# Optimization experiments

Measured on AMD Instinct MI355X. Metric: run time of the kernel, lower is better.

## Reference

```python
import jax, jax.numpy as jnp
import numpy as np

B, S, D, H = 2, 2048, 1024, 16
DK = D // H  # 64
EPS = 1e-10
ROPE_BASE = 500000.0


def _rms_norm(x, w):
    # RMSNorm over last dim: w * x / sqrt(mean(x^2) + eps)
    return w * x * jax.lax.rsqrt(jnp.mean(x * x, axis=-1, keepdims=True) + EPS)


def _rope_tables(seq_len, dk):
    inv_freq = 1.0 / (ROPE_BASE ** (jnp.arange(0, dk, 2, dtype=jnp.float32) / dk))
    t = jnp.arange(seq_len, dtype=jnp.float32)
    freqs = jnp.outer(t, inv_freq)            # (S, dk/2)
    emb = jnp.concatenate([freqs, freqs], -1)  # (S, dk)
    return jnp.cos(emb), jnp.sin(emb)


def _rotate_half(x):
    x1, x2 = jnp.split(x, 2, axis=-1)
    return jnp.concatenate([-x2, x1], axis=-1)


def setup_inputs() -> dict:
    key = jax.random.key(0)
    ks = jax.random.split(key, 8)
    scale = 1.0 / np.sqrt(D)
    return {
        "q": jax.random.normal(ks[0], (B, S, D), jnp.float32),
        "k": jax.random.normal(ks[1], (B, S, D), jnp.float32),
        "v": jax.random.normal(ks[2], (B, S, D), jnp.float32),
        "Wq": jax.random.normal(ks[3], (D, D), jnp.float32) * scale,
        "Wk": jax.random.normal(ks[4], (D, D), jnp.float32) * scale,
        "Wv": jax.random.normal(ks[5], (D, D), jnp.float32) * scale,
        "Wo": jax.random.normal(ks[6], (D, D), jnp.float32) * scale,
        "q_norm_w": jnp.ones((DK,), jnp.float32) + 0.02 * jax.random.normal(ks[7], (DK,), jnp.float32),
        "k_norm_w": jnp.ones((DK,), jnp.float32),
    }


def reference(q, k, v, Wq, Wk, Wv, Wo, q_norm_w, k_norm_w):
    Bq, Sq, _ = q.shape
    # Projections (torch Linear: x @ W.T), split into heads -> (B, H, S, DK)
    def proj(x, W):
        return (x @ W.T).reshape(Bq, Sq, H, DK).transpose(0, 2, 1, 3)
    query, key_, value = proj(q, Wq), proj(k, Wk), proj(v, Wv)
    # Per-head QK RMSNorm
    query = _rms_norm(query, q_norm_w)
    key_ = _rms_norm(key_, k_norm_w)
    # RoPE
    cos, sin = _rope_tables(Sq, DK)  # (S, DK) each; broadcast over (B, H)
    query = query * cos + _rotate_half(query) * sin
    key_ = key_ * cos + _rotate_half(key_) * sin
    # Causal attention
    scale = 1.0 / np.sqrt(DK)
    scores = jnp.einsum("bhqd,bhkd->bhqk", query, key_) * scale
    causal = jnp.tril(jnp.ones((Sq, Sq), bool))
    scores = jnp.where(causal, scores, -jnp.inf)
    probs = jax.nn.softmax(scores, axis=-1)
    attn = jnp.einsum("bhqk,bhkd->bhqd", probs, value)
    # Merge heads and output projection
    attn = attn.transpose(0, 2, 1, 3).reshape(Bq, Sq, D)
    return attn @ Wo.T
```

## Files before the change

kernel.cpp:

```cpp
#include <hip/hip_runtime.h>
#include <hip/hip_bf16.h>
#include <math.h>

#define B_  2
#define S_  2048
#define D_  1024
#define H_  16
#define DK_ 64

typedef __attribute__((ext_vector_type(8))) short bf16x8;
typedef __attribute__((ext_vector_type(4))) float f32x4;

#define MFMA_BF16(a, b, c) __builtin_amdgcn_mfma_f32_16x16x32_bf16((a), (b), (c), 0, 0, 0)

#define QSCALE 0.18033688011112042f
#define ROPE_L2 0.591611512f

__device__ __forceinline__ unsigned short f2bf(float f) {
  unsigned int u = __float_as_uint(f);
  u += 0x7FFFu + ((u >> 16) & 1u);
  return (unsigned short)(u >> 16);
}

__device__ __forceinline__ void gl_lds16(const void* g, void* l) {
  __builtin_amdgcn_global_load_lds(
      (const __attribute__((address_space(1))) void*)g,
      (__attribute__((address_space(3))) void*)l, 16, 0, 0);
}

__device__ __forceinline__ int lsw(int row, int col) {
  return row * 64 + ((((col) >> 3) ^ (row & 7)) << 3) + (col & 7);
}

__global__ __launch_bounds__(256)
void cvt_bf16(const float* __restrict__ q, const float* __restrict__ k,
              const float* __restrict__ v, const float* __restrict__ wq,
              const float* __restrict__ wk, const float* __restrict__ wv,
              const float* __restrict__ wo,
              unsigned short* __restrict__ qb, unsigned short* __restrict__ kb,
              unsigned short* __restrict__ vb, unsigned short* __restrict__ wqb,
              unsigned short* __restrict__ wkb, unsigned short* __restrict__ wvb,
              unsigned short* __restrict__ wob) {
  const float* src; unsigned short* dst; int n;
  switch (blockIdx.y) {
    case 0: src = q;  dst = qb;  n = B_ * S_ * D_; break;
    case 1: src = k;  dst = kb;  n = B_ * S_ * D_; break;
    case 2: src = v;  dst = vb;  n = B_ * S_ * D_; break;
    case 3: src = wq; dst = wqb; n = D_ * D_; break;
    case 4: src = wk; dst = wkb; n = D_ * D_; break;
    case 5: src = wv; dst = wvb; n = D_ * D_; break;
    default: src = wo; dst = wob; n = D_ * D_; break;
  }
  const int i = (blockIdx.x * 256 + threadIdx.x) * 4;
  if (i >= n) return;
  float4 val = *(const float4*)&src[i];
  ushort4 r4;
  r4.x = f2bf(val.x); r4.y = f2bf(val.y); r4.z = f2bf(val.z); r4.w = f2bf(val.w);
  *(ushort4*)&dst[i] = r4;
}

__global__ __launch_bounds__(256)
void gemm_qkv(const unsigned short* __restrict__ qa, const unsigned short* __restrict__ ka,
              const unsigned short* __restrict__ va,
              const unsigned short* __restrict__ wq, const unsigned short* __restrict__ wk,
              const unsigned short* __restrict__ wv,
              unsigned short* __restrict__ Qo, unsigned short* __restrict__ Ko,
              unsigned short* __restrict__ Vto,
              const float* __restrict__ qnw, const float* __restrict__ knw) {
  __shared__ unsigned short As[2][128 * 32];
  __shared__ unsigned short Bs[2][128 * 32];
  const int z = blockIdx.z;
  const unsigned short* A = (z == 0) ? qa : (z == 1) ? ka : va;
  const unsigned short* W = (z == 0) ? wq : (z == 1) ? wk : wv;

  const int t = threadIdx.x, lane = t & 63, wave = t >> 6;
  const int l16 = lane & 15, quad = lane >> 4;
  const int wm = wave >> 1, wn = wave & 1;
  const int m0 = blockIdx.y * 128, j0 = blockIdx.x * 128;

  f32x4 acc[4][4];
#pragma unroll
  for (int i = 0; i < 4; ++i)
#pragma unroll
    for (int j = 0; j < 4; ++j) acc[i][j] = (f32x4)(0.0f);

  auto stage = [&](int kb, int buf) {
#pragma unroll
    for (int i = 0; i < 2; ++i) {
      const int c  = (wave * 2 + i) * 64 + lane;
      const int r  = c >> 2;
      const int co = (c & 3) * 8;
      gl_lds16(&A[(size_t)(m0 + r) * D_ + kb + co], &As[buf][(wave * 2 + i) * 512]);
      gl_lds16(&W[(size_t)(j0 + r) * D_ + kb + co], &Bs[buf][(wave * 2 + i) * 512]);
    }
  };

  stage(0, 0);
  for (int kb = 0; kb < D_; kb += 32) {
    const int buf = (kb >> 5) & 1;
    __syncthreads();
    if (kb + 32 < D_) stage(kb + 32, buf ^ 1);

    bf16x8 af[4], bfr[4];
#pragma unroll
    for (int mi = 0; mi < 4; ++mi)
      af[mi] = *(const bf16x8*)&As[buf][(wm * 64 + mi * 16 + l16) * 32 + quad * 8];
#pragma unroll
    for (int ni = 0; ni < 4; ++ni)
      bfr[ni] = *(const bf16x8*)&Bs[buf][(wn * 64 + ni * 16 + l16) * 32 + quad * 8];
#pragma unroll
    for (int mi = 0; mi < 4; ++mi)
#pragma unroll
      for (int ni = 0; ni < 4; ++ni)
        acc[mi][ni] = MFMA_BF16(af[mi], bfr[ni], acc[mi][ni]);
  }

  const int h = blockIdx.x * 2 + wn;
  if (z == 2) {
#pragma unroll
    for (int mi = 0; mi < 4; ++mi) {
      const int rowb = m0 + wm * 64 + mi * 16 + quad * 4;
      const int b = rowb >> 11, s0 = rowb & (S_ - 1);
#pragma unroll
      for (int ni = 0; ni < 4; ++ni) {
        const int dk = ni * 16 + l16;
        const unsigned int u0 =
            (unsigned int)f2bf(acc[mi][ni][0]) | ((unsigned int)f2bf(acc[mi][ni][1]) << 16);
        const unsigned int u1 =
            (unsigned int)f2bf(acc[mi][ni][2]) | ((unsigned int)f2bf(acc[mi][ni][3]) << 16);
        *(uint2*)&Vto[((size_t)((b * H_ + h) * DK_ + dk)) * S_ + s0] = make_uint2(u0, u1);
      }
    }
  } else {
    unsigned short* out = (z == 0) ? Qo : Ko;
    const float* nw = (z == 0) ? qnw : knw;
    const float sc  = (z == 0) ? QSCALE : 1.0f;
    float wv_[4];
#pragma unroll
    for (int ni = 0; ni < 4; ++ni) wv_[ni] = nw[ni * 16 + l16];
    const float invA = exp2f(-(float)l16 * ROPE_L2);
    const float invB = exp2f(-(float)(16 + l16) * ROPE_L2);
#pragma unroll
    for (int mi = 0; mi < 4; ++mi) {
#pragma unroll
      for (int r = 0; r < 4; ++r) {
        const int rowg = m0 + wm * 64 + mi * 16 + quad * 4 + r;
        const int b = rowg >> 11, s = rowg & (S_ - 1);
        float ss = 0.f;
#pragma unroll
        for (int ni = 0; ni < 4; ++ni) ss += acc[mi][ni][r] * acc[mi][ni][r];
#pragma unroll
        for (int m = 1; m < 16; m <<= 1) ss += __shfl_xor(ss, m);
        const float rms = rsqrtf(ss * (1.0f / DK_) + 1e-10f);
        float xn[4];
#pragma unroll
        for (int ni = 0; ni < 4; ++ni) xn[ni] = wv_[ni] * acc[mi][ni][r] * rms;
        const float fA = (float)s * invA, fB = (float)s * invB;
        const float cA = __cosf(fA) * sc, sA = __sinf(fA) * sc;
        const float cB = __cosf(fB) * sc, sB = __sinf(fB) * sc;
        float o0 = xn[0] * cA - xn[2] * sA;
        float o1 = xn[1] * cB - xn[3] * sB;
        float o2 = xn[2] * cA + xn[0] * sA;
        float o3 = xn[3] * cB + xn[1] * sB;
        const size_t base = ((size_t)(b * H_ + h) * S_ + s) * DK_;
        out[base +  0 + l16] = f2bf(o0);
        out[base + 16 + l16] = f2bf(o1);
        out[base + 32 + l16] = f2bf(o2);
        out[base + 48 + l16] = f2bf(o3);
      }
    }
  }
}

__global__ __launch_bounds__(256)
void flash3(const unsigned short* __restrict__ Q, const unsigned short* __restrict__ K,
            const unsigned short* __restrict__ Vt, unsigned short* __restrict__ Oa) {
  __shared__ unsigned short Ks[2][64 * 64];
  __shared__ unsigned short Vs[2][64 * 64];
  __shared__ unsigned short Ps[64 * 64];
  const int bx = blockIdx.x;
  const int idx = bx >> 5;
  const int qt = (idx < 16) ? idx : (47 - idx);
  const int bh = bx & 31;
  const int t = threadIdx.x, lane = t & 63, wave = t >> 6;
  const int l16 = lane & 15, quad = lane >> 4;
  const size_t hb = (size_t)bh * S_ * DK_;
  const unsigned short* Qh  = Q + hb;
  const unsigned short* Kh  = K + hb;
  const unsigned short* Vth = Vt + hb;

  bf16x8 qf[2];
#pragma unroll
  for (int ks = 0; ks < 2; ++ks)
    qf[ks] = *(const bf16x8*)
      &Qh[(size_t)(qt * 64 + wave * 16 + l16) * DK_ + ks * 32 + quad * 8];

  bf16x8 ones;
#pragma unroll
  for (int j = 0; j < 8; ++j) ones[j] = (short)0x3F80;

  f32x4 o[4], lacc;
  lacc = (f32x4)(0.0f);
#pragma unroll
  for (int ni = 0; ni < 4; ++ni) o[ni] = (f32x4)(0.0f);

  auto stage = [&](int kt, int bufi) {
#pragma unroll
    for (int i = 0; i < 2; ++i) {
      const int rbase = wave * 16 + i * 8;
      const int r = rbase + (lane >> 3);
      const int c = ((lane & 7) ^ (r & 7)) * 8;
      gl_lds16(&Kh[(size_t)(kt * 64 + r) * DK_ + c], &Ks[bufi][rbase * 64]);
      gl_lds16(&Vth[(size_t)r * S_ + kt * 64 + c], &Vs[bufi][rbase * 64]);
    }
  };

  const int nkt = qt + 1;
  stage(0, 0);
  for (int kt = 0; kt < nkt; ++kt) {
    const int buf = kt & 1;
    __syncthreads();
    if (kt + 1 < nkt) stage(kt + 1, buf ^ 1);

    f32x4 sv[4];
#pragma unroll
    for (int kvi = 0; kvi < 4; ++kvi) sv[kvi] = (f32x4)(0.0f);
#pragma unroll
    for (int ks = 0; ks < 2; ++ks) {
      bf16x8 ak[4];
#pragma unroll
      for (int kvi = 0; kvi < 4; ++kvi)
        ak[kvi] = *(const bf16x8*)&Ks[buf][lsw(kvi * 16 + l16, ks * 32 + quad * 8)];
#pragma unroll
      for (int kvi = 0; kvi < 4; ++kvi)
        sv[kvi] = MFMA_BF16(ak[kvi], qf[ks], sv[kvi]);
    }

    float p[4][4];
    if (kt == qt) {
      const int qg = qt * 64 + wave * 16 + l16;
#pragma unroll
      for (int kvi = 0; kvi < 4; ++kvi)
#pragma unroll
        for (int r = 0; r < 4; ++r) {
          float x = sv[kvi][r];
          if ((kt * 64 + kvi * 16 + quad * 4 + r) > qg) x = -INFINITY;
          p[kvi][r] = exp2f(x);
        }
    } else {
#pragma unroll
      for (int kvi = 0; kvi < 4; ++kvi)
#pragma unroll
        for (int r = 0; r < 4; ++r) p[kvi][r] = exp2f(sv[kvi][r]);
    }

#pragma unroll
    for (int kvi = 0; kvi < 4; ++kvi) {
      const unsigned int d0 =
          (__float_as_uint(p[kvi][1]) & 0xFFFF0000u) | (__float_as_uint(p[kvi][0]) >> 16);
      const unsigned int d1 =
          (__float_as_uint(p[kvi][3]) & 0xFFFF0000u) | (__float_as_uint(p[kvi][2]) >> 16);
      *(uint2*)&Ps[lsw(wave * 16 + l16, kvi * 16 + quad * 4)] = make_uint2(d0, d1);
    }
    asm volatile("s_waitcnt lgkmcnt(0)" ::: "memory");

#pragma unroll
    for (int ks = 0; ks < 2; ++ks) {
      bf16x8 ap, bv[4];
      ap = *(const bf16x8*)&Ps[lsw(wave * 16 + l16, ks * 32 + quad * 8)];
#pragma unroll
      for (int ni = 0; ni < 4; ++ni)
        bv[ni] = *(const bf16x8*)&Vs[buf][lsw(ni * 16 + l16, ks * 32 + quad * 8)];
#pragma unroll
      for (int ni = 0; ni < 4; ++ni)
        o[ni] = MFMA_BF16(ap, bv[ni], o[ni]);
      lacc = MFMA_BF16(ap, ones, lacc);
    }
  }

  const int b = bh >> 4, h = bh & 15;
#pragma unroll
  for (int r = 0; r < 4; ++r) {
    const int srow = qt * 64 + wave * 16 + quad * 4 + r;
    const float linv = 1.0f / lacc[r];
#pragma unroll
    for (int ni = 0; ni < 4; ++ni)
      Oa[((size_t)(b * S_ + srow) * H_ + h) * DK_ + ni * 16 + l16] =
          f2bf(o[ni][r] * linv);
  }
}

__global__ __launch_bounds__(256)
void gemm_out(const unsigned short* __restrict__ A, const unsigned short* __restrict__ W,
              float* __restrict__ out) {
  __shared__ unsigned short As[2][128 * 32];
  __shared__ unsigned short Bs[2][128 * 32];
  const int t = threadIdx.x, lane = t & 63, wave = t >> 6;
  const int l16 = lane & 15, quad = lane >> 4;
  const int wm = wave >> 1, wn = wave & 1;
  const int m0 = blockIdx.y * 128, j0 = blockIdx.x * 128;

  f32x4 acc[4][4];
#pragma unroll
  for (int i = 0; i < 4; ++i)
#pragma unroll
    for (int j = 0; j < 4; ++j) acc[i][j] = (f32x4)(0.0f);

  auto stage = [&](int kb, int buf) {
#pragma unroll
    for (int i = 0; i < 2; ++i) {
      const int c  = (wave * 2 + i) * 64 + lane;
      const int r  = c >> 2;
      const int co = (c & 3) * 8;
      gl_lds16(&A[(size_t)(m0 + r) * D_ + kb + co], &As[buf][(wave * 2 + i) * 512]);
      gl_lds16(&W[(size_t)(j0 + r) * D_ + kb + co], &Bs[buf][(wave * 2 + i) * 512]);
    }
  };

  stage(0, 0);
  for (int kb = 0; kb < D_; kb += 32) {
    const int buf = (kb >> 5) & 1;
    __syncthreads();
    if (kb + 32 < D_) stage(kb + 32, buf ^ 1);

    bf16x8 af[4], bfr[4];
#pragma unroll
    for (int mi = 0; mi < 4; ++mi)
      af[mi] = *(const bf16x8*)&As[buf][(wm * 64 + mi * 16 + l16) * 32 + quad * 8];
#pragma unroll
    for (int ni = 0; ni < 4; ++ni)
      bfr[ni] = *(const bf16x8*)&Bs[buf][(wn * 64 + ni * 16 + l16) * 32 + quad * 8];
#pragma unroll
    for (int mi = 0; mi < 4; ++mi)
#pragma unroll
      for (int ni = 0; ni < 4; ++ni)
        acc[mi][ni] = MFMA_BF16(af[mi], bfr[ni], acc[mi][ni]);
  }

#pragma unroll
  for (int mi = 0; mi < 4; ++mi) {
    const int rowb = m0 + wm * 64 + mi * 16 + quad * 4;
#pragma unroll
    for (int ni = 0; ni < 4; ++ni) {
      const int col = j0 + wn * 64 + ni * 16 + l16;
#pragma unroll
      for (int r = 0; r < 4; ++r)
        out[(size_t)(rowb + r) * D_ + col] = acc[mi][ni][r];
    }
  }
}

extern "C" void kernel_launch(void* const* d_in, const int* in_sizes, int n_in,
                              void* d_out, int out_size, void* d_ws, size_t ws_size,
                              hipStream_t stream) {
  (void)in_sizes; (void)n_in; (void)out_size; (void)ws_size;
  const float* q  = (const float*)d_in[0];
  const float* k  = (const float*)d_in[1];
  const float* v  = (const float*)d_in[2];
  const float* Wq = (const float*)d_in[3];
  const float* Wk = (const float*)d_in[4];
  const float* Wv = (const float*)d_in[5];
  const float* Wo = (const float*)d_in[6];
  const float* qw = (const float*)d_in[7];
  const float* kw = (const float*)d_in[8];

  char* ws = (char*)d_ws;
  const size_t MB = 1u << 20;
  unsigned short* qb  = (unsigned short*)(ws + 0 * MB);
  unsigned short* kb  = (unsigned short*)(ws + 8 * MB);
  unsigned short* vb  = (unsigned short*)(ws + 16 * MB);
  unsigned short* wqb = (unsigned short*)(ws + 24 * MB);
  unsigned short* wkb = (unsigned short*)(ws + 26 * MB);
  unsigned short* wvb = (unsigned short*)(ws + 28 * MB);
  unsigned short* wob = (unsigned short*)(ws + 30 * MB);
  unsigned short* Qb  = (unsigned short*)(ws + 32 * MB);
  unsigned short* Kb  = (unsigned short*)(ws + 40 * MB);
  unsigned short* Vtb = (unsigned short*)(ws + 48 * MB);
  unsigned short* Ab  = (unsigned short*)(ws + 56 * MB);

  cvt_bf16<<<dim3(4096, 7), 256, 0, stream>>>(q, k, v, Wq, Wk, Wv, Wo,
                                              qb, kb, vb, wqb, wkb, wvb, wob);

  gemm_qkv<<<dim3(D_ / 128, (B_ * S_) / 128, 3), 256, 0, stream>>>(
      qb, kb, vb, wqb, wkb, wvb, Qb, Kb, Vtb, qw, kw);

  flash3<<<1024, 256, 0, stream>>>(Qb, Kb, Vtb, Ab);

  gemm_out<<<dim3(D_ / 128, (B_ * S_) / 128), 256, 0, stream>>>(Ab, wob, (float*)d_out);
}
```

Measured before the change: 215.3 us.

## Replace LDS-staged GEMM tiles with direct global register double-buffering

Both the QKV and output GEMMs stop staging A/W tiles through shared memory with async global-to-LDS loads and barriers. Each wave now loads its MFMA fragments straight from global memory into two register sets, alternating between them to overlap loads with compute. The launch grid is flattened to 1D with M-tile-fastest ordering, which changes L2 reuse, and launch bounds request 3 blocks per CU. The cost is that fragments are no longer shared within a block, so redundant global/L2 traffic rises and loads become strided 16-byte rows with no coalescing across the tile.

```diff
diff --git a/kernel.cpp b/kernel.cpp
--- a/kernel.cpp
+++ b/kernel.cpp
@@ -59,7 +59,7 @@
   *(ushort4*)&dst[i] = r4;
 }
 
-__global__ __launch_bounds__(256)
+__global__ __launch_bounds__(256, 3)
 void gemm_qkv(const unsigned short* __restrict__ qa, const unsigned short* __restrict__ ka,
               const unsigned short* __restrict__ va,
               const unsigned short* __restrict__ wq, const unsigned short* __restrict__ wk,
@@ -67,16 +67,17 @@
               unsigned short* __restrict__ Qo, unsigned short* __restrict__ Ko,
               unsigned short* __restrict__ Vto,
               const float* __restrict__ qnw, const float* __restrict__ knw) {
-  __shared__ unsigned short As[2][128 * 32];
-  __shared__ unsigned short Bs[2][128 * 32];
-  const int z = blockIdx.z;
+  const int bidx = blockIdx.x;
+  const int by = bidx & 31;
+  const int bxj = (bidx >> 5) & 7;
+  const int z = bidx >> 8;
   const unsigned short* A = (z == 0) ? qa : (z == 1) ? ka : va;
   const unsigned short* W = (z == 0) ? wq : (z == 1) ? wk : wv;
 
   const int t = threadIdx.x, lane = t & 63, wave = t >> 6;
   const int l16 = lane & 15, quad = lane >> 4;
   const int wm = wave >> 1, wn = wave & 1;
-  const int m0 = blockIdx.y * 128, j0 = blockIdx.x * 128;
+  const int m0 = by * 128, j0 = bxj * 128;
 
   f32x4 acc[4][4];
 #pragma unroll
@@ -84,38 +85,34 @@
 #pragma unroll
     for (int j = 0; j < 4; ++j) acc[i][j] = (f32x4)(0.0f);
 
-  auto stage = [&](int kb, int buf) {
-#pragma unroll
-    for (int i = 0; i < 2; ++i) {
-      const int c  = (wave * 2 + i) * 64 + lane;
-      const int r  = c >> 2;
-      const int co = (c & 3) * 8;
-      gl_lds16(&A[(size_t)(m0 + r) * D_ + kb + co], &As[buf][(wave * 2 + i) * 512]);
-      gl_lds16(&W[(size_t)(j0 + r) * D_ + kb + co], &Bs[buf][(wave * 2 + i) * 512]);
-    }
-  };
-
-  stage(0, 0);
-  for (int kb = 0; kb < D_; kb += 32) {
-    const int buf = (kb >> 5) & 1;
-    __syncthreads();
-    if (kb + 32 < D_) stage(kb + 32, buf ^ 1);
-
-    bf16x8 af[4], bfr[4];
+  const unsigned short* Arow = A + (size_t)(m0 + wm * 64 + l16) * D_ + quad * 8;
+  const unsigned short* Wrow = W + (size_t)(j0 + wn * 64 + l16) * D_ + quad * 8;
+
+  bf16x8 a0[4], b0[4], a1[4], b1[4];
+  auto loadf = [&](bf16x8* af, bf16x8* bf, int kb) {
+#pragma unroll
+    for (int i = 0; i < 4; ++i) {
+      af[i] = *(const bf16x8*)(Arow + (size_t)i * 16 * D_ + kb);
+      bf[i] = *(const bf16x8*)(Wrow + (size_t)i * 16 * D_ + kb);
+    }
+  };
+  auto comp = [&](bf16x8* af, bf16x8* bf) {
 #pragma unroll
     for (int mi = 0; mi < 4; ++mi)
-      af[mi] = *(const bf16x8*)&As[buf][(wm * 64 + mi * 16 + l16) * 32 + quad * 8];
-#pragma unroll
-    for (int ni = 0; ni < 4; ++ni)
-      bfr[ni] = *(const bf16x8*)&Bs[buf][(wn * 64 + ni * 16 + l16) * 32 + quad * 8];
-#pragma unroll
-    for (int mi = 0; mi < 4; ++mi)
 #pragma unroll
       for (int ni = 0; ni < 4; ++ni)
-        acc[mi][ni] = MFMA_BF16(af[mi], bfr[ni], acc[mi][ni]);
-  }
-
-  const int h = blockIdx.x * 2 + wn;
+        acc[mi][ni] = MFMA_BF16(af[mi], bf[ni], acc[mi][ni]);
+  };
+
+  loadf(a0, b0, 0);
+  for (int kb = 0; kb < D_; kb += 64) {
+    if (kb + 32 < D_) loadf(a1, b1, kb + 32);
+    comp(a0, b0);
+    if (kb + 64 < D_) loadf(a0, b0, kb + 64);
+    comp(a1, b1);
+  }
+
+  const int h = bxj * 2 + wn;
   if (z == 2) {
 #pragma unroll
     for (int mi = 0; mi < 4; ++mi) {
@@ -290,15 +287,16 @@
   }
 }
 
-__global__ __launch_bounds__(256)
+__global__ __launch_bounds__(256, 3)
 void gemm_out(const unsigned short* __restrict__ A, const unsigned short* __restrict__ W,
               float* __restrict__ out) {
-  __shared__ unsigned short As[2][128 * 32];
-  __shared__ unsigned short Bs[2][128 * 32];
+  const int bidx = blockIdx.x;
+  const int by = bidx & 31;
+  const int bxj = bidx >> 5;
   const int t = threadIdx.x, lane = t & 63, wave = t >> 6;
   const int l16 = lane & 15, quad = lane >> 4;
   const int wm = wave >> 1, wn = wave & 1;
-  const int m0 = blockIdx.y * 128, j0 = blockIdx.x * 128;
+  const int m0 = by * 128, j0 = bxj * 128;
 
   f32x4 acc[4][4];
 #pragma unroll
@@ -306,35 +304,31 @@
 #pragma unroll
     for (int j = 0; j < 4; ++j) acc[i][j] = (f32x4)(0.0f);
 
-  auto stage = [&](int kb, int buf) {
-#pragma unroll
-    for (int i = 0; i < 2; ++i) {
-      const int c  = (wave * 2 + i) * 64 + lane;
-      const int r  = c >> 2;
-      const int co = (c & 3) * 8;
-      gl_lds16(&A[(size_t)(m0 + r) * D_ + kb + co], &As[buf][(wave * 2 + i) * 512]);
-      gl_lds16(&W[(size_t)(j0 + r) * D_ + kb + co], &Bs[buf][(wave * 2 + i) * 512]);
-    }
-  };
-
-  stage(0, 0);
-  for (int kb = 0; kb < D_; kb += 32) {
-    const int buf = (kb >> 5) & 1;
-    __syncthreads();
-    if (kb + 32 < D_) stage(kb + 32, buf ^ 1);
-
-    bf16x8 af[4], bfr[4];
+  const unsigned short* Arow = A + (size_t)(m0 + wm * 64 + l16) * D_ + quad * 8;
+  const unsigned short* Wrow = W + (size_t)(j0 + wn * 64 + l16) * D_ + quad * 8;
+
+  bf16x8 a0[4], b0[4], a1[4], b1[4];
+  auto loadf = [&](bf16x8* af, bf16x8* bf, int kb) {
+#pragma unroll
+    for (int i = 0; i < 4; ++i) {
+      af[i] = *(const bf16x8*)(Arow + (size_t)i * 16 * D_ + kb);
+      bf[i] = *(const bf16x8*)(Wrow + (size_t)i * 16 * D_ + kb);
+    }
+  };
+  auto comp = [&](bf16x8* af, bf16x8* bf) {
 #pragma unroll
     for (int mi = 0; mi < 4; ++mi)
-      af[mi] = *(const bf16x8*)&As[buf][(wm * 64 + mi * 16 + l16) * 32 + quad * 8];
-#pragma unroll
-    for (int ni = 0; ni < 4; ++ni)
-      bfr[ni] = *(const bf16x8*)&Bs[buf][(wn * 64 + ni * 16 + l16) * 32 + quad * 8];
-#pragma unroll
-    for (int mi = 0; mi < 4; ++mi)
 #pragma unroll
       for (int ni = 0; ni < 4; ++ni)
-        acc[mi][ni] = MFMA_BF16(af[mi], bfr[ni], acc[mi][ni]);
+        acc[mi][ni] = MFMA_BF16(af[mi], bf[ni], acc[mi][ni]);
+  };
+
+  loadf(a0, b0, 0);
+  for (int kb = 0; kb < D_; kb += 64) {
+    if (kb + 32 < D_) loadf(a1, b1, kb + 32);
+    comp(a0, b0);
+    if (kb + 64 < D_) loadf(a0, b0, kb + 64);
+    comp(a1, b1);
   }
 
 #pragma unroll
@@ -381,10 +375,9 @@
   cvt_bf16<<<dim3(4096, 7), 256, 0, stream>>>(q, k, v, Wq, Wk, Wv, Wo,
                                               qb, kb, vb, wqb, wkb, wvb, wob);
 
-  gemm_qkv<<<dim3(D_ / 128, (B_ * S_) / 128, 3), 256, 0, stream>>>(
-      qb, kb, vb, wqb, wkb, wvb, Qb, Kb, Vtb, qw, kw);
+  gemm_qkv<<<768, 256, 0, stream>>>(qb, kb, vb, wqb, wkb, wvb, Qb, Kb, Vtb, qw, kw);
 
   flash3<<<1024, 256, 0, stream>>>(Qb, Kb, Vtb, Ab);
 
-  gemm_out<<<dim3(D_ / 128, (B_ * S_) / 128), 256, 0, stream>>>(Ab, wob, (float*)d_out);
-}
+  gemm_out<<<256, 256, 0, stream>>>(Ab, wob, (float*)d_out);
+}
```

Result: slower. 280.0 us (+30.1%).

## Transpose flash score work split across waves and shrink output GEMM tile

Applied to the files above, without the earlier changes.

The attention kernel now has each wave compute scores for its own 16 keys against all 64 queries. Each wave holds all Q fragments in registers and reads a single K fragment from LDS per k-step, cutting LDS traffic for K. Because each wave now needs P values written by other waves, a barrier is added after the P store, which costs synchronisation. Launch bounds now request 4 blocks per SM, and the output GEMM tile is narrowed from 128x128 to 128x64, doubling the grid for better occupancy at the cost of less reuse of the A operand.

```diff
diff --git a/kernel.cpp b/kernel.cpp
--- a/kernel.cpp
+++ b/kernel.cpp
@@ -172,8 +172,8 @@
   }
 }
 
-__global__ __launch_bounds__(256)
-void flash3(const unsigned short* __restrict__ Q, const unsigned short* __restrict__ K,
+__global__ __launch_bounds__(256, 4)
+void flash4(const unsigned short* __restrict__ Q, const unsigned short* __restrict__ K,
             const unsigned short* __restrict__ Vt, unsigned short* __restrict__ Oa) {
   __shared__ unsigned short Ks[2][64 * 64];
   __shared__ unsigned short Vs[2][64 * 64];
@@ -189,11 +189,13 @@
   const unsigned short* Kh  = K + hb;
   const unsigned short* Vth = Vt + hb;
 
-  bf16x8 qf[2];
-#pragma unroll
-  for (int ks = 0; ks < 2; ++ks)
-    qf[ks] = *(const bf16x8*)
-      &Qh[(size_t)(qt * 64 + wave * 16 + l16) * DK_ + ks * 32 + quad * 8];
+  bf16x8 qf[4][2];
+#pragma unroll
+  for (int ni = 0; ni < 4; ++ni)
+#pragma unroll
+    for (int ks = 0; ks < 2; ++ks)
+      qf[ni][ks] = *(const bf16x8*)
+        &Qh[(size_t)(qt * 64 + ni * 16 + l16) * DK_ + ks * 32 + quad * 8];
 
   bf16x8 ones;
 #pragma unroll
@@ -224,45 +226,44 @@
 
     f32x4 sv[4];
 #pragma unroll
-    for (int kvi = 0; kvi < 4; ++kvi) sv[kvi] = (f32x4)(0.0f);
+    for (int ni = 0; ni < 4; ++ni) sv[ni] = (f32x4)(0.0f);
 #pragma unroll
     for (int ks = 0; ks < 2; ++ks) {
-      bf16x8 ak[4];
-#pragma unroll
-      for (int kvi = 0; kvi < 4; ++kvi)
-        ak[kvi] = *(const bf16x8*)&Ks[buf][lsw(kvi * 16 + l16, ks * 32 + quad * 8)];
-#pragma unroll
-      for (int kvi = 0; kvi < 4; ++kvi)
-        sv[kvi] = MFMA_BF16(ak[kvi], qf[ks], sv[kvi]);
+      const bf16x8 ak = *(const bf16x8*)&Ks[buf][lsw(wave * 16 + l16, ks * 32 + quad * 8)];
+#pragma unroll
+      for (int ni = 0; ni < 4; ++ni)
+        sv[ni] = MFMA_BF16(ak, qf[ni][ks], sv[ni]);
     }
 
     float p[4][4];
     if (kt == qt) {
-      const int qg = qt * 64 + wave * 16 + l16;
-#pragma unroll
-      for (int kvi = 0; kvi < 4; ++kvi)
+      const int kvb = kt * 64 + wave * 16 + quad * 4;
+#pragma unroll
+      for (int ni = 0; ni < 4; ++ni) {
+        const int qg = qt * 64 + ni * 16 + l16;
 #pragma unroll
         for (int r = 0; r < 4; ++r) {
-          float x = sv[kvi][r];
-          if ((kt * 64 + kvi * 16 + quad * 4 + r) > qg) x = -INFINITY;
-          p[kvi][r] = exp2f(x);
+          float x = sv[ni][r];
+          if ((kvb + r) > qg) x = -INFINITY;
+          p[ni][r] = exp2f(x);
         }
+      }
     } else {
 #pragma unroll
-      for (int kvi = 0; kvi < 4; ++kvi)
-#pragma unroll
-        for (int r = 0; r < 4; ++r) p[kvi][r] = exp2f(sv[kvi][r]);
-    }
-
-#pragma unroll
-    for (int kvi = 0; kvi < 4; ++kvi) {
+      for (int ni = 0; ni < 4; ++ni)
+#pragma unroll
+        for (int r = 0; r < 4; ++r) p[ni][r] = exp2f(sv[ni][r]);
+    }
+
+#pragma unroll
+    for (int ni = 0; ni < 4; ++ni) {
       const unsigned int d0 =
-          (__float_as_uint(p[kvi][1]) & 0xFFFF0000u) | (__float_as_uint(p[kvi][0]) >> 16);
+          (__float_as_uint(p[ni][1]) & 0xFFFF0000u) | (__float_as_uint(p[ni][0]) >> 16);
       const unsigned int d1 =
-          (__float_as_uint(p[kvi][3]) & 0xFFFF0000u) | (__float_as_uint(p[kvi][2]) >> 16);
-      *(uint2*)&Ps[lsw(wave * 16 + l16, kvi * 16 + quad * 4)] = make_uint2(d0, d1);
-    }
-    asm volatile("s_waitcnt lgkmcnt(0)" ::: "memory");
+          (__float_as_uint(p[ni][3]) & 0xFFFF0000u) | (__float_as_uint(p[ni][2]) >> 16);
+      *(uint2*)&Ps[lsw(ni * 16 + l16, wave * 16 + quad * 4)] = make_uint2(d0, d1);
+    }
+    asm volatile("s_waitcnt lgkmcnt(0)\n\ts_barrier" ::: "memory");
 
 #pragma unroll
     for (int ks = 0; ks < 2; ++ks) {
@@ -294,17 +295,17 @@
 void gemm_out(const unsigned short* __restrict__ A, const unsigned short* __restrict__ W,
               float* __restrict__ out) {
   __shared__ unsigned short As[2][128 * 32];
-  __shared__ unsigned short Bs[2][128 * 32];
+  __shared__ unsigned short Bs[2][64 * 32];
   const int t = threadIdx.x, lane = t & 63, wave = t >> 6;
   const int l16 = lane & 15, quad = lane >> 4;
   const int wm = wave >> 1, wn = wave & 1;
-  const int m0 = blockIdx.y * 128, j0 = blockIdx.x * 128;
-
-  f32x4 acc[4][4];
+  const int m0 = blockIdx.y * 128, j0 = blockIdx.x * 64;
+
+  f32x4 acc[4][2];
 #pragma unroll
   for (int i = 0; i < 4; ++i)
 #pragma unroll
-    for (int j = 0; j < 4; ++j) acc[i][j] = (f32x4)(0.0f);
+    for (int j = 0; j < 2; ++j) acc[i][j] = (f32x4)(0.0f);
 
   auto stage = [&](int kb, int buf) {
 #pragma unroll
@@ -313,7 +314,12 @@
       const int r  = c >> 2;
       const int co = (c & 3) * 8;
       gl_lds16(&A[(size_t)(m0 + r) * D_ + kb + co], &As[buf][(wave * 2 + i) * 512]);
-      gl_lds16(&W[(size_t)(j0 + r) * D_ + kb + co], &Bs[buf][(wave * 2 + i) * 512]);
+    }
+    {
+      const int c  = wave * 64 + lane;
+      const int r  = c >> 2;
+      const int co = (c & 3) * 8;
+      gl_lds16(&W[(size_t)(j0 + r) * D_ + kb + co], &Bs[buf][wave * 512]);
     }
   };
 
@@ -323,17 +329,17 @@
     __syncthreads();
     if (kb + 32 < D_) stage(kb + 32, buf ^ 1);
 
-    bf16x8 af[4], bfr[4];
+    bf16x8 af[4], bfr[2];
 #pragma unroll
     for (int mi = 0; mi < 4; ++mi)
       af[mi] = *(const bf16x8*)&As[buf][(wm * 64 + mi * 16 + l16) * 32 + quad * 8];
 #pragma unroll
-    for (int ni = 0; ni < 4; ++ni)
-      bfr[ni] = *(const bf16x8*)&Bs[buf][(wn * 64 + ni * 16 + l16) * 32 + quad * 8];
+    for (int ni = 0; ni < 2; ++ni)
+      bfr[ni] = *(const bf16x8*)&Bs[buf][(wn * 32 + ni * 16 + l16) * 32 + quad * 8];
 #pragma unroll
     for (int mi = 0; mi < 4; ++mi)
 #pragma unroll
-      for (int ni = 0; ni < 4; ++ni)
+      for (int ni = 0; ni < 2; ++ni)
         acc[mi][ni] = MFMA_BF16(af[mi], bfr[ni], acc[mi][ni]);
   }
 
@@ -341,8 +347,8 @@
   for (int mi = 0; mi < 4; ++mi) {
     const int rowb = m0 + wm * 64 + mi * 16 + quad * 4;
 #pragma unroll
-    for (int ni = 0; ni < 4; ++ni) {
-      const int col = j0 + wn * 64 + ni * 16 + l16;
+    for (int ni = 0; ni < 2; ++ni) {
+      const int col = j0 + wn * 32 + ni * 16 + l16;
 #pragma unroll
       for (int r = 0; r < 4; ++r)
         out[(size_t)(rowb + r) * D_ + col] = acc[mi][ni][r];
@@ -384,7 +390,7 @@
   gemm_qkv<<<dim3(D_ / 128, (B_ * S_) / 128, 3), 256, 0, stream>>>(
       qb, kb, vb, wqb, wkb, wvb, Qb, Kb, Vtb, qw, kw);
 
-  flash3<<<1024, 256, 0, stream>>>(Qb, Kb, Vtb, Ab);
-
-  gemm_out<<<dim3(D_ / 128, (B_ * S_) / 128), 256, 0, stream>>>(Ab, wob, (float*)d_out);
-}
+  flash4<<<1024, 256, 0, stream>>>(Qb, Kb, Vtb, Ab);
+
+  gemm_out<<<dim3(D_ / 64, (B_ * S_) / 128), 256, 0, stream>>>(Ab, wob, (float*)d_out);
+}
```

Result: no change. 218.5 us (+1.5%).
